# Kernel tuning notes

Hardware: AMD Instinct MI355X
Metric: run time of the kernel (lower is better)

## Reference

```python
import jax, jax.numpy as jnp
import numpy as np

N_NODES = 51200
N_EDGES = 614400
ORIG = 92
AFL = 64      # atom_fea_len
NFL = 64      # nbr_fea_len
BINS = 100
N_CONV = 3
EPS = 1e-5


def _bn(h, g, b):
    # BatchNorm1d in training mode: biased batch statistics over dim 0
    mu = h.mean(0)
    var = h.var(0)
    return (h - mu) * jax.lax.rsqrt(var + EPS) * g + b


def setup_inputs() -> dict:
    key = jax.random.key(0)
    ks = jax.random.split(key, 16)
    inp = {
        "x": jax.random.normal(ks[0], (N_NODES, ORIG), dtype=jnp.float32),
        "edge_index": jax.random.randint(ks[1], (2, N_EDGES), 0, N_NODES, dtype=jnp.int32),
        "edge_attr": jax.random.uniform(ks[2], (N_EDGES, 1), dtype=jnp.float32),
        "batchsize": 128,
        # encoder-level params
        "attention": jnp.ones((ORIG,), jnp.float32),
        "emb_W": jax.random.normal(ks[3], (ORIG, AFL), jnp.float32) / np.sqrt(ORIG),
        "emb_b": jnp.zeros((AFL,), jnp.float32),
        # per-conv params stacked along axis 0 (n_conv layers)
        "ad_w1": jax.random.normal(ks[4], (N_CONV, 1, BINS), jnp.float32),
        "ad_b1": jnp.zeros((N_CONV, BINS), jnp.float32),
        "ad_w2": jax.random.normal(ks[5], (N_CONV, BINS, BINS), jnp.float32) / np.sqrt(BINS),
        "ad_b2": jnp.zeros((N_CONV, BINS), jnp.float32),
        "ad_alpha": jax.random.uniform(ks[6], (N_CONV, 1), dtype=jnp.float32),
        "ad_lut": jax.random.uniform(ks[7], (N_CONV, BINS, NFL), dtype=jnp.float32),
        "fc_W": jax.random.normal(ks[8], (N_CONV, 2 * AFL + NFL, 2 * AFL), jnp.float32) / np.sqrt(2 * AFL + NFL),
        "fc_b": jnp.zeros((N_CONV, 2 * AFL), jnp.float32),
        "bn1_g": jnp.ones((N_CONV, 2 * AFL), jnp.float32),
        "bn1_b": jnp.zeros((N_CONV, 2 * AFL), jnp.float32),
        "bn2_g": jnp.ones((N_CONV, AFL), jnp.float32),
        "bn2_b": jnp.zeros((N_CONV, AFL), jnp.float32),
        # pre_pooling linear
        "pp_W": jax.random.normal(ks[9], (AFL, AFL), jnp.float32) / np.sqrt(AFL),
        "pp_b": jnp.zeros((AFL,), jnp.float32),
    }
    return inp


def _cgconv(h, src, dst, edge_attr, w1, b1, w2, b2, alpha, lut, fcW, fcb, g1, be1, g2, be2):
    # AutoDiscretization of the scalar edge feature -> [E, NFL]
    v2 = jax.nn.leaky_relu(edge_attr @ w1 + b1)               # [E, BINS]
    v3 = v2 @ w2 + b2 + alpha * v2                            # [E, BINS]
    e = jax.nn.softmax(v3, axis=-1) @ lut                     # [E, NFL]
    # message: gather endpoints, fused gated MLP (x_i = target, x_j = source)
    z = jnp.concatenate([h[dst], h[src], e], axis=1) @ fcW + fcb  # [E, 2*AFL]
    z = _bn(z, g1, be1)
    nbr_filter, nbr_core = jnp.split(z, 2, axis=1)
    msg = jax.nn.relu(nbr_filter) * jax.nn.relu(nbr_core)     # [E, AFL]
    # aggregate (scatter-add to target nodes) + update
    aggr = jax.ops.segment_sum(msg, dst, num_segments=N_NODES)
    return jax.nn.relu(h + _bn(aggr, g2, be2))


def reference(x, edge_index, edge_attr, batchsize, attention, emb_W, emb_b,
              ad_w1, ad_b1, ad_w2, ad_b2, ad_alpha, ad_lut,
              fc_W, fc_b, bn1_g, bn1_b, bn2_g, bn2_b, pp_W, pp_b):
    src = edge_index[0]  # x_j
    dst = edge_index[1]  # x_i / aggregation target
    num_atom = N_NODES // batchsize

    h = (x * attention) @ emb_W + emb_b                       # [N, AFL]
    feas = [h]
    for l in range(N_CONV):
        h = _cgconv(h, src, dst, edge_attr,
                    ad_w1[l], ad_b1[l], ad_w2[l], ad_b2[l], ad_alpha[l], ad_lut[l],
                    fc_W[l], fc_b[l], bn1_g[l], bn1_b[l], bn2_g[l], bn2_b[l])
        feas.append(h)

    A = jnp.concatenate(feas, axis=0)                         # [(n_conv+1)*N, AFL]
    A = jax.nn.softmax(A @ pp_W + pp_b, axis=1)
    A = A.reshape(N_CONV + 1, batchsize, num_atom, AFL)
    crys_fea = A.sum(axis=0).sum(axis=1)                      # [batchsize, AFL]
    return crys_fea
```

## Files before the change

### kernel.cpp

```cpp
#include <hip/hip_runtime.h>

#define N_NODES 51200
#define N_EDGES 614400
#define ORIG 92
#define AFL 64
#define NFL 64
#define BINS 100
#define NCONV 3
#define BN_EPS 1e-5f
#define NTILES (N_EDGES / 16)
#define NGROUPS (NTILES / 2)

typedef __attribute__((ext_vector_type(8))) short bf8;
typedef __attribute__((ext_vector_type(4))) float f32x4;

__device__ __forceinline__ float bflo(unsigned int u) { return __uint_as_float(u << 16); }
__device__ __forceinline__ float bfhi(unsigned int u) { return __uint_as_float(u & 0xffff0000u); }
__device__ __forceinline__ unsigned int f2bf(float f) {
    unsigned int u = __float_as_uint(f);
    return (u + 0x7fffu + ((u >> 16) & 1u)) >> 16;
}
__device__ __forceinline__ short bfs(float f) { return (short)f2bf(f); }

__global__ __launch_bounds__(256) void hist_kernel(const int* __restrict__ ei,
                                                   int* __restrict__ cnt)
{
    int e = blockIdx.x * 256 + threadIdx.x;
    atomicAdd(&cnt[ei[N_EDGES + e]], 1);
}

__global__ __launch_bounds__(1024) void scan_kernel(int* __restrict__ cnt_cursor,
                                                    int* __restrict__ rowptr)
{
    __shared__ int part[1024];
    const int t = threadIdx.x;
    const int base = t * 50;
    int s = 0;
#pragma unroll 10
    for (int i = 0; i < 50; ++i) s += cnt_cursor[base + i];
    part[t] = s;
    __syncthreads();
    for (int off = 1; off < 1024; off <<= 1) {
        int v = (t >= off) ? part[t - off] : 0;
        __syncthreads();
        part[t] += v;
        __syncthreads();
    }
    int run = (t == 0) ? 0 : part[t - 1];
    for (int i = 0; i < 50; ++i) {
        int c = cnt_cursor[base + i];
        rowptr[base + i] = run;
        cnt_cursor[base + i] = run;
        run += c;
    }
    if (t == 1023) rowptr[N_NODES] = run;
}

__global__ __launch_bounds__(256) void permbuild_kernel(const int* __restrict__ ei,
                                                        int* __restrict__ cursor,
                                                        int* __restrict__ perm)
{
    int e = blockIdx.x * 256 + threadIdx.x;
    int d = ei[N_EDGES + e];
    int pos = atomicAdd(&cursor[d], 1);
    perm[pos] = e;
}

__global__ __launch_bounds__(256) void gather_sorted_kernel(
    const int* __restrict__ perm, const float* __restrict__ ea,
    const int* __restrict__ ei,
    float* __restrict__ ea_s, int* __restrict__ src_s, int* __restrict__ dst_s)
{
    int i = blockIdx.x * 256 + threadIdx.x;
    int e = perm[i];
    ea_s[i] = ea[e];
    src_s[i] = ei[e];
    dst_s[i] = ei[N_EDGES + e];
}

__global__ __launch_bounds__(256) void embed_kernel(
    const float* __restrict__ x, const float* __restrict__ att,
    const float* __restrict__ W, const float* __restrict__ b,
    float* __restrict__ h0, unsigned short* __restrict__ hbf)
{
    const int wave = threadIdx.x >> 6, lane = threadIdx.x & 63;
    const int gw = blockIdx.x * 4 + wave;
    const float bv = b[lane];
    for (int n = gw; n < N_NODES; n += gridDim.x * 4) {
        const float* xr = x + (size_t)n * ORIG;
        float acc = bv;
        for (int k = 0; k < ORIG; ++k)
            acc = fmaf(xr[k] * att[k], W[k * AFL + lane], acc);
        h0[(size_t)n * AFL + lane] = acc;
        hbf[(size_t)n * AFL + lane] = (unsigned short)f2bf(acc);
    }
}

#define SBS 202

__global__ __launch_bounds__(512, 1) void edge_kernel(
    const float* __restrict__ ea_s, const int* __restrict__ src_s,
    const int* __restrict__ dst_s,
    const unsigned short* __restrict__ hbf,
    const float* __restrict__ w1, const float* __restrict__ b1,
    const float* __restrict__ w2, const float* __restrict__ b2,
    const float* __restrict__ alpha_p, const float* __restrict__ lut,
    const float* __restrict__ fcW, const float* __restrict__ fcb,
    short* __restrict__ zo, float* __restrict__ stats)
{
    __shared__ short sW2f[7 * 4 * 64 * 8];
    __shared__ short sLutf[4 * 4 * 64 * 8];
    __shared__ short sFcf[6 * 8 * 64 * 8];
    __shared__ short sBuf[8][16 * SBS];

    const int tid = threadIdx.x;
    for (int i = tid; i < 1792; i += 512) {
        int t = i >> 8, rem = i & 255, s = rem >> 6, le = rem & 63;
        int n = 16 * t + (le & 15);
        int kb = 32 * s + ((le >> 4) << 3);
        short* d = &sW2f[i * 8];
#pragma unroll
        for (int j = 0; j < 8; ++j) {
            int k = kb + j;
            d[j] = bfs((n < BINS && k < BINS) ? w2[k * BINS + n] : 0.f);
        }
    }
    for (int i = tid; i < 1024; i += 512) {
        int t = i >> 8, rem = i & 255, s = rem >> 6, le = rem & 63;
        int n = 16 * t + (le & 15);
        int kb = 32 * s + ((le >> 4) << 3);
        short* d = &sLutf[i * 8];
#pragma unroll
        for (int j = 0; j < 8; ++j) {
            int k = kb + j;
            d[j] = bfs(k < BINS ? lut[k * NFL + n] : 0.f);
        }
    }
    for (int i = tid; i < 3072; i += 512) {
        int s = i >> 9, rem = i & 511, t = rem >> 6, le = rem & 63;
        int n = 16 * t + (le & 15);
        int kb = 32 * s + ((le >> 4) << 3);
        short* d = &sFcf[i * 8];
#pragma unroll
        for (int j = 0; j < 8; ++j)
            d[j] = bfs(fcW[(kb + j) * 128 + n]);
    }
    __syncthreads();

    const int wave = tid >> 6, lane = tid & 63;
    const int ln = lane & 15, q = lane >> 4;
    short* sB = &sBuf[wave][0];
    const float alpha = alpha_p[0];

    float w1c[7], b1c[7], b2c[7];
#pragma unroll
    for (int t = 0; t < 7; ++t) {
        int c = ln + 16 * t;
        bool v = c < BINS;
        w1c[t] = v ? w1[c] : 0.f;
        b1c[t] = v ? b1[c] : 0.f;
        b2c[t] = v ? b2[c] : 0.f;
    }
    float fbias[8];
#pragma unroll
    for (int t = 0; t < 8; ++t) fbias[t] = fcb[ln + 16 * t];

    float ss[8], sq[8];
#pragma unroll
    for (int t = 0; t < 8; ++t) { ss[t] = 0.f; sq[t] = 0.f; }

    int g = blockIdx.x * 8 + wave;
    float avA = 0.f, avB = 0.f;
    int snA = 0, dnA = 0, snB = 0, dnB = 0;
    if (g < NGROUPS) {
        int b0 = g * 32 + ln;
        avA = ea_s[b0];      snA = src_s[b0];      dnA = dst_s[b0];
        avB = ea_s[b0 + 16]; snB = src_s[b0 + 16]; dnB = dst_s[b0 + 16];
    }

    for (; g < NGROUPS; g += 2048) {
        const int ebase = g * 32;
        bf8 hdA[2], hsA[2], hdB[2], hsB[2];
#pragma unroll
        for (int i = 0; i < 2; ++i) {
            int idx = i * 64 + lane;
            int row = idx >> 3, seg = idx & 7;
            int da = __shfl(dnA, row, 64), sa = __shfl(snA, row, 64);
            int db = __shfl(dnB, row, 64), sb2 = __shfl(snB, row, 64);
            hdA[i] = *(const bf8*)&hbf[(size_t)da * 64 + seg * 8];
            hsA[i] = *(const bf8*)&hbf[(size_t)sa * 64 + seg * 8];
            hdB[i] = *(const bf8*)&hbf[(size_t)db * 64 + seg * 8];
            hsB[i] = *(const bf8*)&hbf[(size_t)sb2 * 64 + seg * 8];
        }
        const int gn = g + 2048;
        const int gs = (gn < NGROUPS) ? gn : g;
        const int bN = gs * 32 + ln;
        float avAN = ea_s[bN];      int snAN = src_s[bN];      int dnAN = dst_s[bN];
        float avBN = ea_s[bN + 16]; int snBN = src_s[bN + 16]; int dnBN = dst_s[bN + 16];

        f32x4 accA[7], accB[7];
#pragma unroll
        for (int r = 0; r < 4; ++r) {
            float ar = __shfl(avA, q * 4 + r, 64);
            const int rowoff = (q * 4 + r) * SBS;
#pragma unroll
            for (int t = 0; t < 7; ++t) {
                float v2c = fmaf(ar, w1c[t], b1c[t]);
                v2c = v2c > 0.f ? v2c : 0.01f * v2c;
                accA[t][r] = fmaf(alpha, v2c, b2c[t]);
                if (t < 6 || ln < 4) sB[rowoff + ln + 16 * t] = bfs(v2c);
            }
        }
#pragma unroll
        for (int i = 0; i < 7; ++i) {
            int idx = i * 64 + lane;
            int row = idx / 28, c = 100 + (idx - row * 28);
            sB[row * SBS + c] = 0;
        }
        bf8 aA[4];
#pragma unroll
        for (int s = 0; s < 4; ++s) aA[s] = *(const bf8*)&sB[ln * SBS + 32 * s + 8 * q];
#pragma unroll
        for (int r = 0; r < 4; ++r) {
            float ar = __shfl(avB, q * 4 + r, 64);
            const int rowoff = (q * 4 + r) * SBS;
#pragma unroll
            for (int t = 0; t < 7; ++t) {
                float v2c = fmaf(ar, w1c[t], b1c[t]);
                v2c = v2c > 0.f ? v2c : 0.01f * v2c;
                accB[t][r] = fmaf(alpha, v2c, b2c[t]);
                if (t < 6 || ln < 4) sB[rowoff + ln + 16 * t] = bfs(v2c);
            }
        }
        bf8 aB[4];
#pragma unroll
        for (int s = 0; s < 4; ++s) aB[s] = *(const bf8*)&sB[ln * SBS + 32 * s + 8 * q];
#pragma unroll
        for (int s = 0; s < 4; ++s)
#pragma unroll
            for (int t = 0; t < 7; ++t) {
                bf8 bw = *(const bf8*)&sW2f[((t * 4 + s) * 64 + lane) * 8];
                accA[t] = __builtin_amdgcn_mfma_f32_16x16x32_bf16(aA[s], bw, accA[t], 0, 0, 0);
                accB[t] = __builtin_amdgcn_mfma_f32_16x16x32_bf16(aB[s], bw, accB[t], 0, 0, 0);
            }
#pragma unroll
        for (int r = 0; r < 4; ++r) {
            float evA[7], evB[7], sumA = 0.f, sumB = 0.f;
#pragma unroll
            for (int t = 0; t < 7; ++t) {
                bool on = (t < 6) || (ln < 4);
                evA[t] = on ? __expf(accA[t][r]) : 0.f; sumA += evA[t];
                evB[t] = on ? __expf(accB[t][r]) : 0.f; sumB += evB[t];
            }
#pragma unroll
            for (int o = 8; o >= 1; o >>= 1) {
                sumA += __shfl_xor(sumA, o, 16);
                sumB += __shfl_xor(sumB, o, 16);
            }
            float iA = 1.0f / sumA, iB = 1.0f / sumB;
#pragma unroll
            for (int t = 0; t < 7; ++t) { accA[t][r] = evA[t] * iA; accB[t][r] = evB[t] * iB; }
        }
#pragma unroll
        for (int r = 0; r < 4; ++r)
#pragma unroll
            for (int t = 0; t < 7; ++t)
                if (t < 6 || ln < 4) sB[(q * 4 + r) * SBS + ln + 16 * t] = bfs(accA[t][r]);
        bf8 apA[4];
#pragma unroll
        for (int s = 0; s < 4; ++s) apA[s] = *(const bf8*)&sB[ln * SBS + 32 * s + 8 * q];
#pragma unroll
        for (int r = 0; r < 4; ++r)
#pragma unroll
            for (int t = 0; t < 7; ++t)
                if (t < 6 || ln < 4) sB[(q * 4 + r) * SBS + ln + 16 * t] = bfs(accB[t][r]);
        bf8 apB[4];
#pragma unroll
        for (int s = 0; s < 4; ++s) apB[s] = *(const bf8*)&sB[ln * SBS + 32 * s + 8 * q];
        f32x4 eaccA[4], eaccB[4];
#pragma unroll
        for (int t = 0; t < 4; ++t) {
            eaccA[t] = (f32x4){0.f, 0.f, 0.f, 0.f};
            eaccB[t] = (f32x4){0.f, 0.f, 0.f, 0.f};
        }
#pragma unroll
        for (int s = 0; s < 4; ++s)
#pragma unroll
            for (int t = 0; t < 4; ++t) {
                bf8 bl = *(const bf8*)&sLutf[((t * 4 + s) * 64 + lane) * 8];
                eaccA[t] = __builtin_amdgcn_mfma_f32_16x16x32_bf16(apA[s], bl, eaccA[t], 0, 0, 0);
                eaccB[t] = __builtin_amdgcn_mfma_f32_16x16x32_bf16(apB[s], bl, eaccB[t], 0, 0, 0);
            }
#pragma unroll
        for (int i = 0; i < 2; ++i) {
            int idx = i * 64 + lane;
            int row = idx >> 3, seg = idx & 7;
            *(bf8*)&sB[row * SBS + seg * 8] = hdA[i];
            *(bf8*)&sB[row * SBS + 64 + seg * 8] = hsA[i];
        }
#pragma unroll
        for (int t = 0; t < 4; ++t)
#pragma unroll
            for (int r = 0; r < 4; ++r)
                sB[(q * 4 + r) * SBS + 128 + ln + 16 * t] = bfs(eaccA[t][r]);
        bf8 acA[6];
#pragma unroll
        for (int s = 0; s < 6; ++s) acA[s] = *(const bf8*)&sB[ln * SBS + 32 * s + 8 * q];
#pragma unroll
        for (int i = 0; i < 2; ++i) {
            int idx = i * 64 + lane;
            int row = idx >> 3, seg = idx & 7;
            *(bf8*)&sB[row * SBS + seg * 8] = hdB[i];
            *(bf8*)&sB[row * SBS + 64 + seg * 8] = hsB[i];
        }
#pragma unroll
        for (int t = 0; t < 4; ++t)
#pragma unroll
            for (int r = 0; r < 4; ++r)
                sB[(q * 4 + r) * SBS + 128 + ln + 16 * t] = bfs(eaccB[t][r]);
        bf8 acB[6];
#pragma unroll
        for (int s = 0; s < 6; ++s) acB[s] = *(const bf8*)&sB[ln * SBS + 32 * s + 8 * q];
        f32x4 zaccA[8], zaccB[8];
#pragma unroll
        for (int t = 0; t < 8; ++t) {
            zaccA[t] = (f32x4){fbias[t], fbias[t], fbias[t], fbias[t]};
            zaccB[t] = (f32x4){fbias[t], fbias[t], fbias[t], fbias[t]};
        }
#pragma unroll
        for (int s = 0; s < 6; ++s)
#pragma unroll
            for (int t = 0; t < 8; ++t) {
                bf8 bw = *(const bf8*)&sFcf[((s * 8 + t) * 64 + lane) * 8];
                zaccA[t] = __builtin_amdgcn_mfma_f32_16x16x32_bf16(acA[s], bw, zaccA[t], 0, 0, 0);
                zaccB[t] = __builtin_amdgcn_mfma_f32_16x16x32_bf16(acB[s], bw, zaccB[t], 0, 0, 0);
            }
#pragma unroll
        for (int t = 0; t < 8; ++t)
#pragma unroll
            for (int r = 0; r < 4; ++r) {
                float zv = zaccA[t][r];
                ss[t] += zv; sq[t] = fmaf(zv, zv, sq[t]);
                sB[(q * 4 + r) * SBS + ln + 16 * t] = bfs(zv);
            }
#pragma unroll
        for (int i = 0; i < 4; ++i) {
            int idx = i * 64 + lane;
            int row = idx >> 4, seg = idx & 15;
            bf8 v = *(const bf8*)&sB[row * SBS + seg * 8];
            *(bf8*)&zo[(size_t)(ebase + row) * 128 + seg * 8] = v;
        }
#pragma unroll
        for (int t = 0; t < 8; ++t)
#pragma unroll
            for (int r = 0; r < 4; ++r) {
                float zv = zaccB[t][r];
                ss[t] += zv; sq[t] = fmaf(zv, zv, sq[t]);
                sB[(q * 4 + r) * SBS + ln + 16 * t] = bfs(zv);
            }
#pragma unroll
        for (int i = 0; i < 4; ++i) {
            int idx = i * 64 + lane;
            int row = idx >> 4, seg = idx & 15;
            bf8 v = *(const bf8*)&sB[row * SBS + seg * 8];
            *(bf8*)&zo[(size_t)(ebase + 16 + row) * 128 + seg * 8] = v;
        }
        avA = avAN; snA = snAN; dnA = dnAN;
        avB = avBN; snB = snBN; dnB = dnBN;
    }

#pragma unroll
    for (int t = 0; t < 8; ++t) {
        ss[t] += __shfl_xor(ss[t], 16, 64); ss[t] += __shfl_xor(ss[t], 32, 64);
        sq[t] += __shfl_xor(sq[t], 16, 64); sq[t] += __shfl_xor(sq[t], 32, 64);
    }
    __syncthreads();
    float* sred = (float*)&sBuf[0][0];
    if (q == 0) {
#pragma unroll
        for (int t = 0; t < 8; ++t) {
            sred[wave * 128 + ln + 16 * t] = ss[t];
            sred[1024 + wave * 128 + ln + 16 * t] = sq[t];
        }
    }
    __syncthreads();
    if (tid < 256) {
        int base = (tid < 128) ? 0 : 1024;
        int col = tid & 127;
        float s = 0.f;
#pragma unroll
        for (int w = 0; w < 8; ++w) s += sred[base + w * 128 + col];
        atomicAdd(&stats[tid], s);
    }
}

__global__ void bn_fin_kernel(const float* __restrict__ stats,
                              const float* __restrict__ g, const float* __restrict__ b,
                              float* __restrict__ bnp, int C, float invN)
{
    int c = threadIdx.x;
    if (c >= C) return;
    float mu = stats[c] * invN;
    float var = stats[C + c] * invN - mu * mu;
    float sc = g[c] * rsqrtf(var + BN_EPS);
    bnp[c] = sc;
    bnp[C + c] = b[c] - mu * sc;
}

__global__ __launch_bounds__(256) void aggregate_kernel(
    const unsigned int* __restrict__ z32, const int* __restrict__ rowptr,
    const float* __restrict__ bnp, float* __restrict__ aggr,
    float* __restrict__ stats2)
{
    const int w = threadIdx.x >> 6;
    const int lane = threadIdx.x & 63;
    const int f2 = lane & 31, slot = lane >> 5, f = 2 * f2;
    const float sc0 = bnp[f], sc1 = bnp[f + 1];
    const float sh0 = bnp[128 + f], sh1 = bnp[128 + f + 1];
    const float tc0 = bnp[64 + f], tc1 = bnp[64 + f + 1];
    const float th0 = bnp[192 + f], th1 = bnp[192 + f + 1];
    float s0 = 0.f, s1 = 0.f, q0 = 0.f, q1 = 0.f;
    for (int n = blockIdx.x * 4 + w; n < N_NODES; n += 6400) {
        const int s = rowptr[n], e_end = rowptr[n + 1];
        float a0 = 0.f, a1 = 0.f;
        for (int e = s + slot; e < e_end; e += 2) {
            unsigned int ua = z32[(size_t)e * 64 + f2];
            unsigned int ub = z32[(size_t)e * 64 + 32 + f2];
            float zf0 = fmaf(bflo(ua), sc0, sh0);
            float zf1 = fmaf(bfhi(ua), sc1, sh1);
            float zc0 = fmaf(bflo(ub), tc0, th0);
            float zc1 = fmaf(bfhi(ub), tc1, th1);
            a0 += fmaxf(zf0, 0.f) * fmaxf(zc0, 0.f);
            a1 += fmaxf(zf1, 0.f) * fmaxf(zc1, 0.f);
        }
        a0 += __shfl_xor(a0, 32, 64);
        a1 += __shfl_xor(a1, 32, 64);
        if (slot == 0) {
            float2 o; o.x = a0; o.y = a1;
            *(float2*)&aggr[(size_t)n * 64 + f] = o;
            s0 += a0; s1 += a1;
            q0 = fmaf(a0, a0, q0); q1 = fmaf(a1, a1, q1);
        }
    }
    __shared__ float red[4][128];
    if (slot == 0) {
        red[w][f] = s0; red[w][f + 1] = s1;
        red[w][64 + f] = q0; red[w][64 + f + 1] = q1;
    }
    __syncthreads();
    if (threadIdx.x < 128) {
        int c = threadIdx.x;
        float v = red[0][c] + red[1][c] + red[2][c] + red[3][c];
        atomicAdd(&stats2[c], v);
    }
}

__global__ __launch_bounds__(256) void update_kernel(
    const float* __restrict__ h, const float* __restrict__ aggr,
    const float* __restrict__ bnp, float* __restrict__ hout,
    unsigned short* __restrict__ hbf)
{
    int t = blockIdx.x * 256 + threadIdx.x;
    int f = t & 63;
    float v = fmaf(aggr[t], bnp[f], bnp[64 + f]);
    float r = fmaxf(h[t] + v, 0.f);
    hout[t] = r;
    hbf[t] = (unsigned short)f2bf(r);
}

__global__ __launch_bounds__(256) void pool_kernel(
    const float* __restrict__ hbuf, const float* __restrict__ ppW,
    const float* __restrict__ ppb, float* __restrict__ out)
{
    const int l = blockIdx.x >> 7, b = blockIdx.x & 127;
    const int wave = threadIdx.x >> 6, lane = threadIdx.x & 63;
    float wcol[64];
#pragma unroll
    for (int k = 0; k < 64; ++k) wcol[k] = ppW[k * 64 + lane];
    const float bias = ppb[lane];
    const float* base = hbuf + ((size_t)l * N_NODES + (size_t)b * 400) * 64;
    __shared__ float srow[4][2][64];
    __shared__ float sacc[4][64];
    float acc = 0.f;
    for (int r = wave * 2; r < 400; r += 8) {
        srow[wave][0][lane] = base[(size_t)r * 64 + lane];
        srow[wave][1][lane] = base[(size_t)r * 64 + 64 + lane];
        float lg0 = bias, lg1 = bias;
#pragma unroll
        for (int k4 = 0; k4 < 64; k4 += 4) {
            float4 a = *(const float4*)&srow[wave][0][k4];
            float4 c = *(const float4*)&srow[wave][1][k4];
            lg0 = fmaf(a.x, wcol[k4 + 0], lg0); lg1 = fmaf(c.x, wcol[k4 + 0], lg1);
            lg0 = fmaf(a.y, wcol[k4 + 1], lg0); lg1 = fmaf(c.y, wcol[k4 + 1], lg1);
            lg0 = fmaf(a.z, wcol[k4 + 2], lg0); lg1 = fmaf(c.z, wcol[k4 + 2], lg1);
            lg0 = fmaf(a.w, wcol[k4 + 3], lg0); lg1 = fmaf(c.w, wcol[k4 + 3], lg1);
        }
        float m0 = lg0, m1 = lg1;
#pragma unroll
        for (int o = 32; o >= 1; o >>= 1) {
            m0 = fmaxf(m0, __shfl_xor(m0, o, 64));
            m1 = fmaxf(m1, __shfl_xor(m1, o, 64));
        }
        float e0 = __expf(lg0 - m0), e1 = __expf(lg1 - m1);
        float s0 = e0, s1 = e1;
#pragma unroll
        for (int o = 32; o >= 1; o >>= 1) {
            s0 += __shfl_xor(s0, o, 64);
            s1 += __shfl_xor(s1, o, 64);
        }
        acc += e0 * (1.0f / s0) + e1 * (1.0f / s1);
    }
    sacc[wave][lane] = acc;
    __syncthreads();
    if (wave == 0) {
        float t = sacc[0][lane] + sacc[1][lane] + sacc[2][lane] + sacc[3][lane];
        atomicAdd(&out[(size_t)b * 64 + lane], t);
    }
}

extern "C" void kernel_launch(void* const* d_in, const int* in_sizes, int n_in,
                              void* d_out, int out_size, void* d_ws, size_t ws_size,
                              hipStream_t stream)
{
    const float* x        = (const float*)d_in[0];
    const int*   ei       = (const int*)d_in[1];
    const float* ea       = (const float*)d_in[2];
    const float* att      = (const float*)d_in[4];
    const float* embW     = (const float*)d_in[5];
    const float* embB     = (const float*)d_in[6];
    const float* ad_w1    = (const float*)d_in[7];
    const float* ad_b1    = (const float*)d_in[8];
    const float* ad_w2    = (const float*)d_in[9];
    const float* ad_b2    = (const float*)d_in[10];
    const float* ad_alpha = (const float*)d_in[11];
    const float* ad_lut   = (const float*)d_in[12];
    const float* fc_W     = (const float*)d_in[13];
    const float* fc_b     = (const float*)d_in[14];
    const float* bn1_g    = (const float*)d_in[15];
    const float* bn1_b    = (const float*)d_in[16];
    const float* bn2_g    = (const float*)d_in[17];
    const float* bn2_b    = (const float*)d_in[18];
    const float* ppW      = (const float*)d_in[19];
    const float* ppb      = (const float*)d_in[20];
    float* out = (float*)d_out;

    char* ws = (char*)d_ws;
    float* hbuf   = (float*)ws;
    short* zU     = (short*)(ws + 52428800);
    float* aggr   = (float*)(ws + 209715200);
    float* stats1 = (float*)(ws + 222822400);
    float* bnp1   = stats1 + 256;
    float* stats2 = bnp1 + 256;
    float* bnp2   = stats2 + 128;
    int*   rowptr = (int*)(ws + 222826496);
    int*   cursor = (int*)(ws + 223031360);
    float* ea_s   = (float*)(ws + 223236160);
    int*   src_s  = (int*)(ws + 225693760);
    int*   dst_s  = (int*)(ws + 228151360);
    int*   perm   = (int*)(ws + 230608960);
    unsigned short* hbf = (unsigned short*)(ws + 230608960);

    hipMemsetAsync(cursor, 0, N_NODES * sizeof(int), stream);
    hist_kernel<<<N_EDGES / 256, 256, 0, stream>>>(ei, cursor);
    scan_kernel<<<1, 1024, 0, stream>>>(cursor, rowptr);
    permbuild_kernel<<<N_EDGES / 256, 256, 0, stream>>>(ei, cursor, perm);
    gather_sorted_kernel<<<N_EDGES / 256, 256, 0, stream>>>(perm, ea, ei, ea_s, src_s, dst_s);

    hipMemsetAsync(out, 0, 128 * 64 * sizeof(float), stream);
    embed_kernel<<<512, 256, 0, stream>>>(x, att, embW, embB, hbuf, hbf);

    for (int l = 0; l < NCONV; ++l) {
        float* h  = hbuf + (size_t)l * N_NODES * AFL;
        float* hn = h + (size_t)N_NODES * AFL;
        hipMemsetAsync(stats1, 0, 768 * 4, stream);
        edge_kernel<<<256, 512, 0, stream>>>(
            ea_s, src_s, dst_s, hbf,
            ad_w1 + l * BINS, ad_b1 + l * BINS,
            ad_w2 + l * BINS * BINS, ad_b2 + l * BINS,
            ad_alpha + l, ad_lut + l * BINS * NFL,
            fc_W + l * 192 * 128, fc_b + l * 128,
            zU, stats1);
        bn_fin_kernel<<<1, 128, 0, stream>>>(stats1, bn1_g + l * 128, bn1_b + l * 128,
                                             bnp1, 128, 1.0f / N_EDGES);
        aggregate_kernel<<<1600, 256, 0, stream>>>((const unsigned int*)zU, rowptr, bnp1,
                                                   aggr, stats2);
        bn_fin_kernel<<<1, 128, 0, stream>>>(stats2, bn2_g + l * 64, bn2_b + l * 64,
                                             bnp2, 64, 1.0f / N_NODES);
        update_kernel<<<N_NODES * 64 / 256, 256, 0, stream>>>(h, aggr, bnp2, hn, hbf);
    }

    pool_kernel<<<512, 256, 0, stream>>>(hbuf, ppW, ppb, out);
}
```

Measured before the change: 1.248 ms.

## Build MFMA operands in registers and split node aggregation from column stats

In the edge kernel, the first-layer discretization activations are now computed straight into MFMA A-operand registers from shared w1/b1 vectors. Gathered node feature rows are likewise loaded straight in fragment layout. This removes the LDS staging round trips for the v2 tile and the h_dst/h_src rows. The aggregate kernel now uses one wave per node with no grid-stride loop, and the BN2 column statistics move to a separate colstats kernel. That adds an extra read pass over aggr and one more launch per layer.

```diff
diff --git a/kernel.cpp b/kernel.cpp
--- a/kernel.cpp
+++ b/kernel.cpp
@@ -111,6 +111,7 @@
     __shared__ short sW2f[7 * 4 * 64 * 8];
     __shared__ short sLutf[4 * 4 * 64 * 8];
     __shared__ short sFcf[6 * 8 * 64 * 8];
+    __shared__ float sW1[128], sB1v[128];
     __shared__ short sBuf[8][16 * SBS];
 
     const int tid = threadIdx.x;
@@ -144,6 +145,10 @@
 #pragma unroll
         for (int j = 0; j < 8; ++j)
             d[j] = bfs(fcW[(kb + j) * 128 + n]);
+    }
+    if (tid < 128) {
+        sW1[tid]  = (tid < BINS) ? w1[tid] : 0.f;
+        sB1v[tid] = (tid < BINS) ? b1[tid] : 0.f;
     }
     __syncthreads();
 
@@ -180,36 +185,81 @@
 
     for (; g < NGROUPS; g += 2048) {
         const int ebase = g * 32;
-        bf8 hdA[2], hsA[2], hdB[2], hsB[2];
-#pragma unroll
-        for (int i = 0; i < 2; ++i) {
-            int idx = i * 64 + lane;
-            int row = idx >> 3, seg = idx & 7;
-            int da = __shfl(dnA, row, 64), sa = __shfl(snA, row, 64);
-            int db = __shfl(dnB, row, 64), sb2 = __shfl(snB, row, 64);
-            hdA[i] = *(const bf8*)&hbf[(size_t)da * 64 + seg * 8];
-            hsA[i] = *(const bf8*)&hbf[(size_t)sa * 64 + seg * 8];
-            hdB[i] = *(const bf8*)&hbf[(size_t)db * 64 + seg * 8];
-            hsB[i] = *(const bf8*)&hbf[(size_t)sb2 * 64 + seg * 8];
-        }
+        bf8 acA[6], acB[6];
+        acA[0] = *(const bf8*)&hbf[(size_t)dnA * 64 + 8 * q];
+        acA[1] = *(const bf8*)&hbf[(size_t)dnA * 64 + 32 + 8 * q];
+        acA[2] = *(const bf8*)&hbf[(size_t)snA * 64 + 8 * q];
+        acA[3] = *(const bf8*)&hbf[(size_t)snA * 64 + 32 + 8 * q];
+        acB[0] = *(const bf8*)&hbf[(size_t)dnB * 64 + 8 * q];
+        acB[1] = *(const bf8*)&hbf[(size_t)dnB * 64 + 32 + 8 * q];
+        acB[2] = *(const bf8*)&hbf[(size_t)snB * 64 + 8 * q];
+        acB[3] = *(const bf8*)&hbf[(size_t)snB * 64 + 32 + 8 * q];
         const int gn = g + 2048;
         const int gs = (gn < NGROUPS) ? gn : g;
         const int bN = gs * 32 + ln;
         float avAN = ea_s[bN];      int snAN = src_s[bN];      int dnAN = dst_s[bN];
         float avBN = ea_s[bN + 16]; int snBN = src_s[bN + 16]; int dnBN = dst_s[bN + 16];
 
+        bf8 aA[4], aB[4];
+#pragma unroll
+        for (int s = 0; s < 4; ++s) {
+            const int kb = 32 * s + 8 * q;
+            float4 w0 = *(const float4*)&sW1[kb];
+            float4 w4 = *(const float4*)&sW1[kb + 4];
+            float4 c0 = *(const float4*)&sB1v[kb];
+            float4 c4 = *(const float4*)&sB1v[kb + 4];
+            float wk[8] = {w0.x, w0.y, w0.z, w0.w, w4.x, w4.y, w4.z, w4.w};
+            float ck[8] = {c0.x, c0.y, c0.z, c0.w, c4.x, c4.y, c4.z, c4.w};
+#pragma unroll
+            for (int j = 0; j < 8; ++j) {
+                float vA = fmaf(avA, wk[j], ck[j]);
+                vA = vA > 0.f ? vA : 0.01f * vA;
+                aA[s][j] = bfs(vA);
+                float vB = fmaf(avB, wk[j], ck[j]);
+                vB = vB > 0.f ? vB : 0.01f * vB;
+                aB[s][j] = bfs(vB);
+            }
+        }
         f32x4 accA[7], accB[7];
 #pragma unroll
         for (int r = 0; r < 4; ++r) {
-            float ar = __shfl(avA, q * 4 + r, 64);
-            const int rowoff = (q * 4 + r) * SBS;
+            float arA = __shfl(avA, q * 4 + r, 64);
+            float arB = __shfl(avB, q * 4 + r, 64);
 #pragma unroll
             for (int t = 0; t < 7; ++t) {
-                float v2c = fmaf(ar, w1c[t], b1c[t]);
-                v2c = v2c > 0.f ? v2c : 0.01f * v2c;
-                accA[t][r] = fmaf(alpha, v2c, b2c[t]);
-                if (t < 6 || ln < 4) sB[rowoff + ln + 16 * t] = bfs(v2c);
-            }
+                float vA = fmaf(arA, w1c[t], b1c[t]);
+                vA = vA > 0.f ? vA : 0.01f * vA;
+                accA[t][r] = fmaf(alpha, vA, b2c[t]);
+                float vB = fmaf(arB, w1c[t], b1c[t]);
+                vB = vB > 0.f ? vB : 0.01f * vB;
+                accB[t][r] = fmaf(alpha, vB, b2c[t]);
+            }
+        }
+#pragma unroll
+        for (int s = 0; s < 4; ++s)
+#pragma unroll
+            for (int t = 0; t < 7; ++t) {
+                bf8 bw = *(const bf8*)&sW2f[((t * 4 + s) * 64 + lane) * 8];
+                accA[t] = __builtin_amdgcn_mfma_f32_16x16x32_bf16(aA[s], bw, accA[t], 0, 0, 0);
+                accB[t] = __builtin_amdgcn_mfma_f32_16x16x32_bf16(aB[s], bw, accB[t], 0, 0, 0);
+            }
+#pragma unroll
+        for (int r = 0; r < 4; ++r) {
+            float evA[7], evB[7], sumA = 0.f, sumB = 0.f;
+#pragma unroll
+            for (int t = 0; t < 7; ++t) {
+                bool on = (t < 6) || (ln < 4);
+                evA[t] = on ? __expf(accA[t][r]) : 0.f; sumA += evA[t];
+                evB[t] = on ? __expf(accB[t][r]) : 0.f; sumB += evB[t];
+            }
+#pragma unroll
+            for (int o = 8; o >= 1; o >>= 1) {
+                sumA += __shfl_xor(sumA, o, 16);
+                sumB += __shfl_xor(sumB, o, 16);
+            }
+            float iA = 1.0f / sumA, iB = 1.0f / sumB;
+#pragma unroll
+            for (int t = 0; t < 7; ++t) { accA[t][r] = evA[t] * iA; accB[t][r] = evB[t] * iB; }
         }
 #pragma unroll
         for (int i = 0; i < 7; ++i) {
@@ -217,50 +267,6 @@
             int row = idx / 28, c = 100 + (idx - row * 28);
             sB[row * SBS + c] = 0;
         }
-        bf8 aA[4];
-#pragma unroll
-        for (int s = 0; s < 4; ++s) aA[s] = *(const bf8*)&sB[ln * SBS + 32 * s + 8 * q];
-#pragma unroll
-        for (int r = 0; r < 4; ++r) {
-            float ar = __shfl(avB, q * 4 + r, 64);
-            const int rowoff = (q * 4 + r) * SBS;
-#pragma unroll
-            for (int t = 0; t < 7; ++t) {
-                float v2c = fmaf(ar, w1c[t], b1c[t]);
-                v2c = v2c > 0.f ? v2c : 0.01f * v2c;
-                accB[t][r] = fmaf(alpha, v2c, b2c[t]);
-                if (t < 6 || ln < 4) sB[rowoff + ln + 16 * t] = bfs(v2c);
-            }
-        }
-        bf8 aB[4];
-#pragma unroll
-        for (int s = 0; s < 4; ++s) aB[s] = *(const bf8*)&sB[ln * SBS + 32 * s + 8 * q];
-#pragma unroll
-        for (int s = 0; s < 4; ++s)
-#pragma unroll
-            for (int t = 0; t < 7; ++t) {
-                bf8 bw = *(const bf8*)&sW2f[((t * 4 + s) * 64 + lane) * 8];
-                accA[t] = __builtin_amdgcn_mfma_f32_16x16x32_bf16(aA[s], bw, accA[t], 0, 0, 0);
-                accB[t] = __builtin_amdgcn_mfma_f32_16x16x32_bf16(aB[s], bw, accB[t], 0, 0, 0);
-            }
-#pragma unroll
-        for (int r = 0; r < 4; ++r) {
-            float evA[7], evB[7], sumA = 0.f, sumB = 0.f;
-#pragma unroll
-            for (int t = 0; t < 7; ++t) {
-                bool on = (t < 6) || (ln < 4);
-                evA[t] = on ? __expf(accA[t][r]) : 0.f; sumA += evA[t];
-                evB[t] = on ? __expf(accB[t][r]) : 0.f; sumB += evB[t];
-            }
-#pragma unroll
-            for (int o = 8; o >= 1; o >>= 1) {
-                sumA += __shfl_xor(sumA, o, 16);
-                sumB += __shfl_xor(sumB, o, 16);
-            }
-            float iA = 1.0f / sumA, iB = 1.0f / sumB;
-#pragma unroll
-            for (int t = 0; t < 7; ++t) { accA[t][r] = evA[t] * iA; accB[t][r] = evB[t] * iB; }
-        }
 #pragma unroll
         for (int r = 0; r < 4; ++r)
 #pragma unroll
@@ -292,35 +298,19 @@
                 eaccB[t] = __builtin_amdgcn_mfma_f32_16x16x32_bf16(apB[s], bl, eaccB[t], 0, 0, 0);
             }
 #pragma unroll
-        for (int i = 0; i < 2; ++i) {
-            int idx = i * 64 + lane;
-            int row = idx >> 3, seg = idx & 7;
-            *(bf8*)&sB[row * SBS + seg * 8] = hdA[i];
-            *(bf8*)&sB[row * SBS + 64 + seg * 8] = hsA[i];
-        }
-#pragma unroll
         for (int t = 0; t < 4; ++t)
 #pragma unroll
             for (int r = 0; r < 4; ++r)
                 sB[(q * 4 + r) * SBS + 128 + ln + 16 * t] = bfs(eaccA[t][r]);
-        bf8 acA[6];
-#pragma unroll
-        for (int s = 0; s < 6; ++s) acA[s] = *(const bf8*)&sB[ln * SBS + 32 * s + 8 * q];
-#pragma unroll
-        for (int i = 0; i < 2; ++i) {
-            int idx = i * 64 + lane;
-            int row = idx >> 3, seg = idx & 7;
-            *(bf8*)&sB[row * SBS + seg * 8] = hdB[i];
-            *(bf8*)&sB[row * SBS + 64 + seg * 8] = hsB[i];
-        }
+        acA[4] = *(const bf8*)&sB[ln * SBS + 128 + 8 * q];
+        acA[5] = *(const bf8*)&sB[ln * SBS + 160 + 8 * q];
 #pragma unroll
         for (int t = 0; t < 4; ++t)
 #pragma unroll
             for (int r = 0; r < 4; ++r)
                 sB[(q * 4 + r) * SBS + 128 + ln + 16 * t] = bfs(eaccB[t][r]);
-        bf8 acB[6];
-#pragma unroll
-        for (int s = 0; s < 6; ++s) acB[s] = *(const bf8*)&sB[ln * SBS + 32 * s + 8 * q];
+        acB[4] = *(const bf8*)&sB[ln * SBS + 128 + 8 * q];
+        acB[5] = *(const bf8*)&sB[ln * SBS + 160 + 8 * q];
         f32x4 zaccA[8], zaccB[8];
 #pragma unroll
         for (int t = 0; t < 8; ++t) {
@@ -409,49 +399,52 @@
 
 __global__ __launch_bounds__(256) void aggregate_kernel(
     const unsigned int* __restrict__ z32, const int* __restrict__ rowptr,
-    const float* __restrict__ bnp, float* __restrict__ aggr,
-    float* __restrict__ stats2)
-{
-    const int w = threadIdx.x >> 6;
+    const float* __restrict__ bnp, float* __restrict__ aggr)
+{
+    const int n = blockIdx.x * 4 + (threadIdx.x >> 6);
     const int lane = threadIdx.x & 63;
     const int f2 = lane & 31, slot = lane >> 5, f = 2 * f2;
     const float sc0 = bnp[f], sc1 = bnp[f + 1];
     const float sh0 = bnp[128 + f], sh1 = bnp[128 + f + 1];
     const float tc0 = bnp[64 + f], tc1 = bnp[64 + f + 1];
     const float th0 = bnp[192 + f], th1 = bnp[192 + f + 1];
-    float s0 = 0.f, s1 = 0.f, q0 = 0.f, q1 = 0.f;
-    for (int n = blockIdx.x * 4 + w; n < N_NODES; n += 6400) {
-        const int s = rowptr[n], e_end = rowptr[n + 1];
-        float a0 = 0.f, a1 = 0.f;
-        for (int e = s + slot; e < e_end; e += 2) {
-            unsigned int ua = z32[(size_t)e * 64 + f2];
-            unsigned int ub = z32[(size_t)e * 64 + 32 + f2];
-            float zf0 = fmaf(bflo(ua), sc0, sh0);
-            float zf1 = fmaf(bfhi(ua), sc1, sh1);
-            float zc0 = fmaf(bflo(ub), tc0, th0);
-            float zc1 = fmaf(bfhi(ub), tc1, th1);
-            a0 += fmaxf(zf0, 0.f) * fmaxf(zc0, 0.f);
-            a1 += fmaxf(zf1, 0.f) * fmaxf(zc1, 0.f);
-        }
-        a0 += __shfl_xor(a0, 32, 64);
-        a1 += __shfl_xor(a1, 32, 64);
-        if (slot == 0) {
-            float2 o; o.x = a0; o.y = a1;
-            *(float2*)&aggr[(size_t)n * 64 + f] = o;
-            s0 += a0; s1 += a1;
-            q0 = fmaf(a0, a0, q0); q1 = fmaf(a1, a1, q1);
-        }
-    }
-    __shared__ float red[4][128];
+    const int s = rowptr[n], e_end = rowptr[n + 1];
+    float a0 = 0.f, a1 = 0.f;
+    for (int e = s + slot; e < e_end; e += 2) {
+        unsigned int ua = z32[(size_t)e * 64 + f2];
+        unsigned int ub = z32[(size_t)e * 64 + 32 + f2];
+        float zf0 = fmaf(bflo(ua), sc0, sh0);
+        float zf1 = fmaf(bfhi(ua), sc1, sh1);
+        float zc0 = fmaf(bflo(ub), tc0, th0);
+        float zc1 = fmaf(bfhi(ub), tc1, th1);
+        a0 += fmaxf(zf0, 0.f) * fmaxf(zc0, 0.f);
+        a1 += fmaxf(zf1, 0.f) * fmaxf(zc1, 0.f);
+    }
+    a0 += __shfl_xor(a0, 32, 64);
+    a1 += __shfl_xor(a1, 32, 64);
     if (slot == 0) {
-        red[w][f] = s0; red[w][f + 1] = s1;
-        red[w][64 + f] = q0; red[w][64 + f + 1] = q1;
-    }
+        float2 w; w.x = a0; w.y = a1;
+        *(float2*)&aggr[(size_t)n * 64 + f] = w;
+    }
+}
+
+__global__ __launch_bounds__(256) void colstats64_kernel(
+    const float* __restrict__ x, int rows, float* __restrict__ stats)
+{
+    int f = threadIdx.x & 63, sub = threadIdx.x >> 6;
+    float s = 0.f, q = 0.f;
+    for (int r = blockIdx.x * 4 + sub; r < rows; r += gridDim.x * 4) {
+        float v = x[(size_t)r * 64 + f];
+        s += v; q = fmaf(v, v, q);
+    }
+    __shared__ float ls[4][64], lq[4][64];
+    ls[sub][f] = s; lq[sub][f] = q;
     __syncthreads();
-    if (threadIdx.x < 128) {
-        int c = threadIdx.x;
-        float v = red[0][c] + red[1][c] + red[2][c] + red[3][c];
-        atomicAdd(&stats2[c], v);
+    if (sub == 0) {
+        s = ls[0][f] + ls[1][f] + ls[2][f] + ls[3][f];
+        q = lq[0][f] + lq[1][f] + lq[2][f] + lq[3][f];
+        atomicAdd(&stats[f], s);
+        atomicAdd(&stats[64 + f], q);
     }
 }
 
@@ -582,8 +575,9 @@
             zU, stats1);
         bn_fin_kernel<<<1, 128, 0, stream>>>(stats1, bn1_g + l * 128, bn1_b + l * 128,
                                              bnp1, 128, 1.0f / N_EDGES);
-        aggregate_kernel<<<1600, 256, 0, stream>>>((const unsigned int*)zU, rowptr, bnp1,
-                                                   aggr, stats2);
+        aggregate_kernel<<<N_NODES / 4, 256, 0, stream>>>((const unsigned int*)zU, rowptr,
+                                                          bnp1, aggr);
+        colstats64_kernel<<<256, 256, 0, stream>>>(aggr, N_NODES, stats2);
         bn_fin_kernel<<<1, 128, 0, stream>>>(stats2, bn2_g + l * 64, bn2_b + l * 64,
                                              bnp2, 64, 1.0f / N_NODES);
         update_kernel<<<N_NODES * 64 / 256, 256, 0, stream>>>(h, aggr, bnp2, hn, hbf);
```

Result: faster. 1.137 ms (-8.9%).
